# Optimization experiments

Hardware: AMD Instinct MI355X
Metric: run time of the kernel (lower is better)

## Reference

```python
import jax, jax.numpy as jnp
import numpy as np


def _ramp_filter(H):
    # skimage-style Fourier ramp filter: 2*|f| with f = fftfreq(H)
    f = np.fft.fftfreq(H)
    return (2.0 * np.abs(f)).astype(np.float32)


def setup_inputs() -> dict:
    key = jax.random.key(0)
    N, H_in, W_in, D_out = 8, 768, 360, 512
    radon_image = jax.random.normal(key, (N, 1, H_in, W_in), dtype=jnp.float32)
    hG = jnp.asarray(_ramp_filter(H_in)).reshape(1, 1, H_in, 1)
    return {"radon_image": radon_image, "hG": hG, "D_out": D_out}


def reference(radon_image, hG, D_out):
    N, _, H, W = radon_image.shape
    D = D_out
    # --- Fourier-domain ramp filtering (2D FFT, multiply by real filter along detector axis, real ifft) ---
    X = jnp.fft.fft2(radon_image[:, 0])                     # [N, H, W] complex
    h = hG[0, 0, :, 0]                                      # [H]
    filt = jnp.real(jnp.fft.ifft2(X * h[None, :, None])).astype(radon_image.dtype)  # [N, H, W]

    # --- backprojection grids (matches np.mgrid / tG construction) ---
    Xg, Yg = jnp.meshgrid(jnp.arange(D), jnp.arange(D), indexing="ij")
    xpr = (Xg - D // 2).astype(jnp.float32)
    ypr = (Yg - D // 2).astype(jnp.float32)
    th = (jnp.pi / 180.0) * jnp.linspace(0.0, 180.0, W, endpoint=False)  # [W]
    txs = -1.0 + jnp.arange(W, dtype=jnp.float32) * (2.0 / (W - 1))     # [W]

    hH = H // 2
    sy = (H - 1) / 2.0   # align_corners=True y scale
    sx = (W - 1) / 2.0   # align_corners=True x scale

    def body(recon, angle):
        th_i, tx_i = angle
        t = ypr * jnp.cos(th_i) - xpr * jnp.sin(th_i)       # [D, D]
        py = (t / hH + 1.0) * sy                            # pixel y coords [D, D]
        px = (tx_i + 1.0) * sx                              # scalar pixel x coord
        x0 = jnp.floor(px).astype(jnp.int32)
        wx = px - x0
        y0 = jnp.floor(py).astype(jnp.int32)
        wy = py - y0

        def samp_col(xi):
            vx = ((xi >= 0) & (xi < W)).astype(filt.dtype)
            col = filt[:, :, jnp.clip(xi, 0, W - 1)]        # [N, H]

            def samp_y(yi):
                vy = ((yi >= 0) & (yi < H)).astype(filt.dtype)
                return col[:, jnp.clip(yi, 0, H - 1)] * vy  # [N, D, D] zero-padded

            v = samp_y(y0) * (1.0 - wy) + samp_y(y0 + 1) * wy
            return v * vx

        val = samp_col(x0) * (1.0 - wx) + samp_col(x0 + 1) * wx  # [N, D, D]
        return recon + val, None

    recon0 = jnp.zeros((N, D, D), dtype=radon_image.dtype)
    recon, _ = jax.lax.scan(body, recon0, (th, txs))
    return (recon * (jnp.pi / (2.0 * W)))[:, None]          # [N, 1, D, D]
```

## Files before the change

kernel.cpp:

```cpp
#include <hip/hip_runtime.h>
#include <math.h>

#define N_IMG 8
#define H 768
#define W 360
#define D 512
#define SY 383.5f
#define SC 0.00436332312998582394f
#define NC 24
#define IPAD 384

typedef __fp16 h2 __attribute__((ext_vector_type(2)));
typedef short short8 __attribute__((ext_vector_type(8)));
typedef float f32x4 __attribute__((ext_vector_type(4)));

__device__ inline unsigned bf16pair(float a, float b) {
    unsigned ua = __builtin_bit_cast(unsigned, a);
    unsigned ub = __builtin_bit_cast(unsigned, b);
    ua += 0x7FFFu + ((ua >> 16) & 1u);
    ub += 0x7FFFu + ((ub >> 16) & 1u);
    return (ua >> 16) | (ub & 0xFFFF0000u);
}

__global__ void build_g_kernel(const float* __restrict__ hG, float* __restrict__ g) {
    int m = blockIdx.x;
    int lane = threadIdx.x;
    float s = 0.f;
#pragma unroll
    for (int q = 0; q < 12; ++q) {
        int k = lane + 64 * q;
        int prod = (k * m) % H;
        float angr = (float)prod * 0.00818123086872313911f;
        s += hG[k] * cosf(angr);
    }
#pragma unroll
    for (int off = 32; off > 0; off >>= 1) s += __shfl_down(s, off);
    if (lane == 0) g[m] = s * (1.0f / (float)H);
}

#define KSTEPS 10

__global__ void build_angbg_kernel(const float* __restrict__ g, uint4* __restrict__ Bg,
                                   float2* __restrict__ ang) {
    int b = blockIdx.x;
    int t = threadIdx.x;
    if (b < 40) {
        int idx = b * 64 + t;
        int L  = idx & 63;
        int tj = idx >> 6;
        int nn = (tj & 3) * 16 + (L & 15);
        int kb = (tj >> 2) * 32 + (L >> 4) * 8;
        float bf[8];
#pragma unroll
        for (int s = 0; s < 8; ++s) {
            int d = nn + 128 - (kb + s);
            d += (d < 0) ? H : 0;
            bf[s] = g[d];
        }
        Bg[idx] = (uint4){bf16pair(bf[0], bf[1]), bf16pair(bf[2], bf[3]),
                          bf16pair(bf[4], bf[5]), bf16pair(bf[6], bf[7])};
    } else {
#pragma unroll
        for (int q = 0; q < 6; ++q) {
            int i = t + 64 * q;
            if (i < W) {
                float th = (float)i * 0.00872664625997164788f;
                float r = SY / 384.0f;
                ang[i] = make_float2(cosf(th) * r, -sinf(th) * r);
            }
        }
    }
}

__global__ __launch_bounds__(256)
void build_rc_kernel(const float* __restrict__ radon, uint4* __restrict__ rcC,
                     float4* __restrict__ out4) {
    __shared__ float xs[32][65];

    const int i0 = blockIdx.x * 64;
    const int c  = blockIdx.y;
    const int n  = blockIdx.z;
    const int tid = threadIdx.x;

    {
        int flat = ((n * NC) + c) * 6 + blockIdx.x;
        if (flat < 1024) {
            out4[flat * 512 + tid]       = make_float4(0.f, 0.f, 0.f, 0.f);
            out4[flat * 512 + 256 + tid] = make_float4(0.f, 0.f, 0.f, 0.f);
        }
    }

    {
        int mr    = tid >> 3;
        int lane8 = tid & 7;
        int ib = i0 + lane8 * 8;
        const float* src = radon + ((size_t)n * H + 32 * c + mr) * W + ib;
        float4 v0, v1;
        if (ib + 7 < W) {
            v0 = *(const float4*)src;
            v1 = *(const float4*)(src + 4);
        } else {
            v0 = make_float4(0.f, 0.f, 0.f, 0.f);
            v1 = make_float4(0.f, 0.f, 0.f, 0.f);
        }
        *(float4*)&xs[mr][lane8 * 8]     = v0;
        *(float4*)&xs[mr][lane8 * 8 + 4] = v1;
    }
    __syncthreads();

    const int il  = tid >> 2;
    const int oct = tid & 3;
    float v[8];
#pragma unroll
    for (int s = 0; s < 8; ++s) v[s] = xs[oct * 8 + s][il];
    uint4 pk = {bf16pair(v[0], v[1]), bf16pair(v[2], v[3]),
                bf16pair(v[4], v[5]), bf16pair(v[6], v[7])};
    rcC[(((size_t)n * NC + c) * IPAD + i0 + il) * 4 + oct] = pk;
}

__global__ __launch_bounds__(256)
void filt_gemm_kernel(const uint4* __restrict__ rcC, const uint4* __restrict__ Bg,
                      unsigned short* __restrict__ colp) {
    __shared__ _Float16 lx[16][64][4];

    const int grp = blockIdx.z;
    const int i0 = blockIdx.y * 16;
    const int y0 = blockIdx.x * 64;
    const int wv = threadIdx.x >> 6;
    const int L  = threadIdx.x & 63;

    const int c0 = (y0 / 32 + 20) % NC;
    const uint4* An = rcC + (size_t)(grp * 4 + wv) * NC * IPAD * 4;
    const int arow = i0 + (L & 15);
    const int aoff = L >> 4;

    f32x4 acc[4];
#pragma unroll
    for (int j = 0; j < 4; ++j) acc[j] = (f32x4){0.f, 0.f, 0.f, 0.f};

    for (int t = 0; t < KSTEPS; ++t) {
        int c = c0 + t;
        c -= (c >= NC) ? NC : 0;
        short8 a = __builtin_bit_cast(short8, An[((size_t)c * IPAD + arow) * 4 + aoff]);
#pragma unroll
        for (int j = 0; j < 4; ++j) {
            short8 b = __builtin_bit_cast(short8, Bg[(t * 4 + j) * 64 + L]);
            acc[j] = __builtin_amdgcn_mfma_f32_16x16x32_bf16(a, b, acc[j], 0, 0, 0);
        }
    }

#pragma unroll
    for (int j = 0; j < 4; ++j) {
#pragma unroll
        for (int r = 0; r < 4; ++r) {
            int ilc = (L >> 4) * 4 + r;
            int ylc = j * 16 + (L & 15);
            lx[ilc][ylc][wv] = (_Float16)(acc[j][r] * SC);
        }
    }
    __syncthreads();

#pragma unroll
    for (int k = 0; k < 4; ++k) {
        int e = threadIdx.x + k * 256;
        int ilc = e >> 6, ylc = e & 63;
        int ig = i0 + ilc;
        if (ig < W) {
            uint2 v = *(const uint2*)&lx[ilc][ylc][0];
            *(uint2*)&colp[((size_t)ig * H + y0 + ylc) * 8 + grp * 4] = v;
        }
    }
}

__global__ __launch_bounds__(512, 6)
void backproj_kernel(const uint4* __restrict__ colp8,
                     const float2* __restrict__ angv, float* __restrict__ outb) {
    __shared__ __align__(16) uint4 colh[2][H];

    const int bid = blockIdx.x;
    const int aq  = bid & 7;
    const int tle = bid >> 3;
    const int a0 = aq * (W / 8);
    const int u0 = (tle >> 3) * 32;
    const int v0 = (tle & 7) * 64;
    const int tid = threadIdx.x;
    const int lane = tid & 63;
    const int tu = tid >> 6;

    const float vf = (float)(v0 + lane - D / 2);
    float uf[4];
#pragma unroll
    for (int r = 0; r < 4; ++r) uf[r] = (float)(u0 + tu + 8 * r - D / 2);

    const h2 hz = {(__fp16)0.f, (__fp16)0.f};
    float acc[4][8];
    h2 hacc[4][4];
#pragma unroll
    for (int r = 0; r < 4; ++r) {
#pragma unroll
        for (int nn = 0; nn < 8; ++nn) acc[r][nn] = 0.f;
#pragma unroll
        for (int p = 0; p < 4; ++p) hacc[r][p] = hz;
    }

    const int y1 = tid;
    const int y2 = tid + 512;

    {
        const size_t ab = (size_t)a0 * H;
        colh[0][y1] = colp8[ab + y1];
        if (tid < 256) colh[0][y2] = colp8[ab + y2];
    }
    __syncthreads();

    for (int j = 0; j < W / 8; ++j) {
        int a = a0 + j;
        int an = (j + 1 < W / 8) ? (a + 1) : a;
        const size_t ab = (size_t)an * H;
        uint4 d = colp8[ab + y1];
        uint4 e = make_uint4(0u, 0u, 0u, 0u);
        if (tid < 256) e = colp8[ab + y2];

        const int cb2 = j & 1;
        float2 AB = angv[a];
        float base = fmaf(vf, AB.x, SY);
#pragma unroll
        for (int r = 0; r < 4; ++r) {
            float py = fmaf(uf[r], AB.y, base);
            float wy = __builtin_amdgcn_fractf(py);
            int iy = (int)py;
            uint4 lo4 = colh[cb2][iy];
            uint4 hi4 = colh[cb2][iy + 1];
            h2 wy2 = __builtin_amdgcn_cvt_pkrtz(wy, wy);
            {
                h2 lo = __builtin_bit_cast(h2, lo4.x), hi = __builtin_bit_cast(h2, hi4.x);
                hacc[r][0] += lo + wy2 * (hi - lo);
            }
            {
                h2 lo = __builtin_bit_cast(h2, lo4.y), hi = __builtin_bit_cast(h2, hi4.y);
                hacc[r][1] += lo + wy2 * (hi - lo);
            }
            {
                h2 lo = __builtin_bit_cast(h2, lo4.z), hi = __builtin_bit_cast(h2, hi4.z);
                hacc[r][2] += lo + wy2 * (hi - lo);
            }
            {
                h2 lo = __builtin_bit_cast(h2, lo4.w), hi = __builtin_bit_cast(h2, hi4.w);
                hacc[r][3] += lo + wy2 * (hi - lo);
            }
        }

        if ((j & 15) == 15) {
#pragma unroll
            for (int r = 0; r < 4; ++r) {
#pragma unroll
                for (int p = 0; p < 4; ++p) {
                    acc[r][2 * p]     += (float)hacc[r][p].x;
                    acc[r][2 * p + 1] += (float)hacc[r][p].y;
                    hacc[r][p] = hz;
                }
            }
        }

        colh[cb2 ^ 1][y1] = d;
        if (tid < 256) colh[cb2 ^ 1][y2] = e;
        __syncthreads();
    }

#pragma unroll
    for (int r = 0; r < 4; ++r) {
#pragma unroll
        for (int p = 0; p < 4; ++p) {
            acc[r][2 * p]     += (float)hacc[r][p].x;
            acc[r][2 * p + 1] += (float)hacc[r][p].y;
        }
        int u = u0 + tu + 8 * r;
#pragma unroll
        for (int nn = 0; nn < 8; ++nn) {
            size_t idx = ((size_t)nn * D + u) * D + v0 + lane;
            atomicAdd(&outb[idx], acc[r][nn]);
        }
    }
}

extern "C" void kernel_launch(void* const* d_in, const int* in_sizes, int n_in,
                              void* d_out, int out_size, void* d_ws, size_t ws_size,
                              hipStream_t stream) {
    const float* radon = (const float*)d_in[0];
    const float* hG    = (const float*)d_in[1];
    float* out = (float*)d_out;

    float*  g    = (float*)d_ws;
    float2* ang  = (float2*)((char*)d_ws + 4096);
    uint4*  Bg   = (uint4*)((char*)d_ws + 8192);
    unsigned short* colp = (unsigned short*)((char*)d_ws + 65536);
    uint4*  rcC  = (uint4*)((char*)d_ws + 4489216);

    build_g_kernel<<<H, 64, 0, stream>>>(hG, g);
    build_angbg_kernel<<<41, 64, 0, stream>>>(g, Bg, ang);
    build_rc_kernel<<<dim3(6, NC, N_IMG), 256, 0, stream>>>(radon, rcC, (float4*)out);
    filt_gemm_kernel<<<dim3(H / 64, 23, 2), 256, 0, stream>>>(rcC, Bg, colp);
    backproj_kernel<<<1024, 512, 0, stream>>>((const uint4*)colp, ang, out);
}
```

Before: 168.3 us.

## Merge filter GEMM image groups into 512-thread blocks; split backprojection lerp accumulators

The filter GEMM now handles all 8 images in one 512-thread block instead of two 256-thread blocks indexed by z. Each output row is then written as a single 16-byte uint4 instead of two 8-byte halves. In the backprojection inner loop, the lerp lo + w*(hi-lo) becomes two independent packed-half accumulations lo*w1 and hi*w2, which shortens the dependency chain. The cost is twice the half-precision accumulator registers, which could lower occupancy under the 6-waves launch bound.

```diff
diff --git a/kernel.cpp b/kernel.cpp
--- a/kernel.cpp
+++ b/kernel.cpp
@@ -118,19 +118,18 @@
     rcC[(((size_t)n * NC + c) * IPAD + i0 + il) * 4 + oct] = pk;
 }
 
-__global__ __launch_bounds__(256)
+__global__ __launch_bounds__(512)
 void filt_gemm_kernel(const uint4* __restrict__ rcC, const uint4* __restrict__ Bg,
-                      unsigned short* __restrict__ colp) {
-    __shared__ _Float16 lx[16][64][4];
-
-    const int grp = blockIdx.z;
+                      uint4* __restrict__ colp8) {
+    __shared__ _Float16 lx[16][64][8];
+
     const int i0 = blockIdx.y * 16;
     const int y0 = blockIdx.x * 64;
     const int wv = threadIdx.x >> 6;
     const int L  = threadIdx.x & 63;
 
     const int c0 = (y0 / 32 + 20) % NC;
-    const uint4* An = rcC + (size_t)(grp * 4 + wv) * NC * IPAD * 4;
+    const uint4* An = rcC + (size_t)wv * NC * IPAD * 4;
     const int arow = i0 + (L & 15);
     const int aoff = L >> 4;
 
@@ -161,13 +160,12 @@
     __syncthreads();
 
 #pragma unroll
-    for (int k = 0; k < 4; ++k) {
-        int e = threadIdx.x + k * 256;
+    for (int k = 0; k < 2; ++k) {
+        int e = threadIdx.x + k * 512;
         int ilc = e >> 6, ylc = e & 63;
         int ig = i0 + ilc;
         if (ig < W) {
-            uint2 v = *(const uint2*)&lx[ilc][ylc][0];
-            *(uint2*)&colp[((size_t)ig * H + y0 + ylc) * 8 + grp * 4] = v;
+            colp8[(size_t)ig * H + y0 + ylc] = *(const uint4*)&lx[ilc][ylc][0];
         }
     }
 }
@@ -193,14 +191,15 @@
     for (int r = 0; r < 4; ++r) uf[r] = (float)(u0 + tu + 8 * r - D / 2);
 
     const h2 hz = {(__fp16)0.f, (__fp16)0.f};
+    const h2 hone = {(__fp16)1.f, (__fp16)1.f};
     float acc[4][8];
-    h2 hacc[4][4];
+    h2 haccL[4][4], haccH[4][4];
 #pragma unroll
     for (int r = 0; r < 4; ++r) {
 #pragma unroll
         for (int nn = 0; nn < 8; ++nn) acc[r][nn] = 0.f;
 #pragma unroll
-        for (int p = 0; p < 4; ++p) hacc[r][p] = hz;
+        for (int p = 0; p < 4; ++p) { haccL[r][p] = hz; haccH[r][p] = hz; }
     }
 
     const int y1 = tid;
@@ -231,22 +230,23 @@
             int iy = (int)py;
             uint4 lo4 = colh[cb2][iy];
             uint4 hi4 = colh[cb2][iy + 1];
-            h2 wy2 = __builtin_amdgcn_cvt_pkrtz(wy, wy);
+            h2 w2 = __builtin_amdgcn_cvt_pkrtz(wy, wy);
+            h2 w1 = hone - w2;
             {
                 h2 lo = __builtin_bit_cast(h2, lo4.x), hi = __builtin_bit_cast(h2, hi4.x);
-                hacc[r][0] += lo + wy2 * (hi - lo);
+                haccL[r][0] += lo * w1;  haccH[r][0] += hi * w2;
             }
             {
                 h2 lo = __builtin_bit_cast(h2, lo4.y), hi = __builtin_bit_cast(h2, hi4.y);
-                hacc[r][1] += lo + wy2 * (hi - lo);
+                haccL[r][1] += lo * w1;  haccH[r][1] += hi * w2;
             }
             {
                 h2 lo = __builtin_bit_cast(h2, lo4.z), hi = __builtin_bit_cast(h2, hi4.z);
-                hacc[r][2] += lo + wy2 * (hi - lo);
+                haccL[r][2] += lo * w1;  haccH[r][2] += hi * w2;
             }
             {
                 h2 lo = __builtin_bit_cast(h2, lo4.w), hi = __builtin_bit_cast(h2, hi4.w);
-                hacc[r][3] += lo + wy2 * (hi - lo);
+                haccL[r][3] += lo * w1;  haccH[r][3] += hi * w2;
             }
         }
 
@@ -255,9 +255,10 @@
             for (int r = 0; r < 4; ++r) {
 #pragma unroll
                 for (int p = 0; p < 4; ++p) {
-                    acc[r][2 * p]     += (float)hacc[r][p].x;
-                    acc[r][2 * p + 1] += (float)hacc[r][p].y;
-                    hacc[r][p] = hz;
+                    acc[r][2 * p]     += (float)haccL[r][p].x + (float)haccH[r][p].x;
+                    acc[r][2 * p + 1] += (float)haccL[r][p].y + (float)haccH[r][p].y;
+                    haccL[r][p] = hz;
+                    haccH[r][p] = hz;
                 }
             }
         }
@@ -271,8 +272,8 @@
     for (int r = 0; r < 4; ++r) {
 #pragma unroll
         for (int p = 0; p < 4; ++p) {
-            acc[r][2 * p]     += (float)hacc[r][p].x;
-            acc[r][2 * p + 1] += (float)hacc[r][p].y;
+            acc[r][2 * p]     += (float)haccL[r][p].x + (float)haccH[r][p].x;
+            acc[r][2 * p + 1] += (float)haccL[r][p].y + (float)haccH[r][p].y;
         }
         int u = u0 + tu + 8 * r;
 #pragma unroll
@@ -293,12 +294,12 @@
     float*  g    = (float*)d_ws;
     float2* ang  = (float2*)((char*)d_ws + 4096);
     uint4*  Bg   = (uint4*)((char*)d_ws + 8192);
-    unsigned short* colp = (unsigned short*)((char*)d_ws + 65536);
+    uint4*  colp8 = (uint4*)((char*)d_ws + 65536);
     uint4*  rcC  = (uint4*)((char*)d_ws + 4489216);
 
     build_g_kernel<<<H, 64, 0, stream>>>(hG, g);
     build_angbg_kernel<<<41, 64, 0, stream>>>(g, Bg, ang);
     build_rc_kernel<<<dim3(6, NC, N_IMG), 256, 0, stream>>>(radon, rcC, (float4*)out);
-    filt_gemm_kernel<<<dim3(H / 64, 23, 2), 256, 0, stream>>>(rcC, Bg, colp);
-    backproj_kernel<<<1024, 512, 0, stream>>>((const uint4*)colp, ang, out);
-}
+    filt_gemm_kernel<<<dim3(H / 64, 23), 512, 0, stream>>>(rcC, Bg, colp8);
+    backproj_kernel<<<1024, 512, 0, stream>>>(colp8, ang, out);
+}
```

After: 192.4 us. 14.3% more time.
